# Kernel optimization log

Measured on AMD Instinct MI355X. Metric: run time of the kernel, lower is better.

Reference implementation:

```python
import jax, jax.numpy as jnp
import numpy as np

NUM_HEAD = 8
ATTN_DIM = 512
WINDOW_WIDTH = 31
HALF_WIN = WINDOW_WIDTH // 2  # symmetric band half-width
NEG_INF = -1e10


def setup_inputs() -> dict:
    key = jax.random.key(0)
    k0, k1, k2 = jax.random.split(key, 3)
    n, c, w = 4, 512, 2048
    out_dim = 512
    input_ = jax.random.normal(k0, (n, c, 1, w), dtype=jnp.float32)
    mask = jnp.ones((n, w), dtype=jnp.float32)  # 1 = valid key position
    # xavier-uniform-like init for the two linears, zero bias (as in the module)
    lim_in = np.sqrt(6.0 / (c + 3 * ATTN_DIM)).astype(np.float32)
    W_in = jax.random.uniform(k1, (3 * ATTN_DIM, c), jnp.float32, -lim_in, lim_in)
    b_in = jnp.zeros((3 * ATTN_DIM,), jnp.float32)
    lim_fc = np.sqrt(6.0 / (ATTN_DIM + out_dim)).astype(np.float32)
    W_fc = jax.random.uniform(k2, (out_dim, ATTN_DIM), jnp.float32, -lim_fc, lim_fc)
    b_fc = jnp.zeros((out_dim,), jnp.float32)
    return {"input_": input_, "mask": mask, "W_in": W_in, "b_in": b_in,
            "W_fc": W_fc, "b_fc": b_fc}


def reference(input_, mask, W_in, b_in, W_fc, b_fc):
    n, c, h, w = input_.shape  # h == 1
    d = ATTN_DIM // NUM_HEAD
    x = input_.reshape(n, c, w).transpose(0, 2, 1)          # [n, w, c]
    temp = x @ W_in.T + b_in                                # [n, w, 3A]
    temp = temp.transpose(0, 2, 1)                          # [n, 3A, w]
    # channel layout after chunk(num_head) then chunk(3): [h, {q,k,v}, d]
    qkv = temp.reshape(n, NUM_HEAD, 3, d, w)
    q, k, v = qkv[:, :, 0], qkv[:, :, 1], qkv[:, :, 2]      # each [n, H, d, w]
    scale = NUM_HEAD / ATTN_DIM                              # == 1/d_head
    attn = jnp.einsum('nhdi,nhdj->nhij', q, k) * scale       # [n, H, w, w]
    # windowed band mask combined with per-key padding mask (clip_mask/mha_mask)
    idx = jnp.arange(w)
    band = jnp.abs(idx[:, None] - idx[None, :]) <= HALF_WIN  # [w, w]
    valid = band[None, None, :, :] & (mask > 0.5)[:, None, None, :]
    attn = jnp.where(valid, attn, NEG_INF)                   # pre-softmax mask
    attn = jax.nn.softmax(attn, axis=-1)
    attn = jnp.where(valid, attn, 0.0)                       # post-softmax mask
    # dropout in eval mode (identity) for a deterministic reference
    out = jnp.einsum('nhdj,nhij->nhdi', v, attn)             # [n, H, d, w]
    out = out.reshape(n, ATTN_DIM, w).transpose(0, 2, 1)     # [n, w, A]
    out = out @ W_fc.T + b_fc                                # [n, w, out_dim]
    od = out.shape[-1]
    return out.transpose(0, 2, 1).reshape(n, od, 1, w)
```

## Files before the change

kernel.cpp:

```cpp
#include <hip/hip_runtime.h>
#include <hip/hip_bf16.h>
#include <math.h>

#define W_SEQ   2048
#define C_IN    512
#define N_BATCH 4
#define NHEAD   8
#define QKV_CH  1536
#define OUT_CH  512
#define ATTND   512
#define N1_4    (QKV_CH * C_IN / 4)
#define N2_4    (OUT_CH * ATTND / 4)

typedef __attribute__((ext_vector_type(8))) short bf16x8;
typedef __attribute__((ext_vector_type(8))) unsigned short u16x8;
typedef __attribute__((ext_vector_type(4))) float f32x4;

__device__ __forceinline__ void gld16(const void* g, void* l) {
    __builtin_amdgcn_global_load_lds((const __attribute__((address_space(1))) void*)g,
                                     (__attribute__((address_space(3))) void*)l, 16, 0, 0);
}
__device__ __forceinline__ unsigned short f2bf(float f) {
    unsigned u = __float_as_uint(f);
    return (unsigned short)((u + 0x7FFFu + ((u >> 16) & 1u)) >> 16);
}

__device__ __forceinline__ void grid_sync(unsigned* bar, unsigned target) {
    __syncthreads();
    if (threadIdx.x == 0) {
        __threadfence();
        atomicAdd(bar, 1u);
        while (atomicAdd(bar, 0u) < target)
            __builtin_amdgcn_s_sleep(8);
        __threadfence();
    }
    __syncthreads();
}

__device__ __forceinline__ void prep_unit(char* sm, int b,
    const float* __restrict__ input, unsigned short* __restrict__ Xh,
    const float* __restrict__ W_in, unsigned short* __restrict__ Winh,
    const float* __restrict__ W_fc, unsigned short* __restrict__ Wfch)
{
    const int t = threadIdx.x;
    float (*ts)[65] = (float(*)[65])sm;
    const int n  = b >> 8, rm = b & 255;
    const int i0 = (rm & 31) * 64, c0 = (rm >> 5) * 64;
    const int tx = t & 63, ty = t >> 6;
    #pragma unroll
    for (int s = 0; s < 16; ++s) {
        const int c = s * 4 + ty;
        ts[c][tx] = input[((size_t)(n * C_IN + c0 + c)) * W_SEQ + i0 + tx];
    }
    __syncthreads();
    const int c8 = t & 7, il = t >> 3;
    #pragma unroll
    for (int s = 0; s < 2; ++s) {
        const int i = il + 32 * s;
        u16x8 hv;
        #pragma unroll
        for (int e = 0; e < 8; ++e) hv[e] = f2bf(ts[c8 * 8 + e][i]);
        *(u16x8*)(&Xh[((size_t)(n * W_SEQ + i0 + i)) * C_IN + c0 + c8 * 8]) = hv;
    }
    const int idx = b * 256 + t;
    if (idx < N1_4) {
        const float4 v = ((const float4*)W_in)[idx];
        ushort4 hh; hh.x = f2bf(v.x); hh.y = f2bf(v.y); hh.z = f2bf(v.z); hh.w = f2bf(v.w);
        ((ushort4*)Winh)[idx] = hh;
    } else {
        const int j = idx - N1_4;
        const float4 v = ((const float4*)W_fc)[j];
        ushort4 hh; hh.x = f2bf(v.x); hh.y = f2bf(v.y); hh.z = f2bf(v.z); hh.w = f2bf(v.w);
        ((ushort4*)Wfch)[j] = hh;
    }
}

template<int EPI>
__device__ __forceinline__ void gemm_body(char* sm, int bx, int by,
    const unsigned short* __restrict__ A, const unsigned short* __restrict__ B,
    const float* __restrict__ bias, void* __restrict__ Cv, const int ldc)
{
    const int t = threadIdx.x;
    const int l = t & 63, w = t >> 6;
    const int m0 = by * 128, n0 = bx * 128;
    const int wm = w >> 1, wn = w & 1;

    const int subrow = l >> 3;
    const int swz    = ((l & 7) ^ subrow) << 4;
    const char* pA = (const char*)A + (size_t)m0 * 1024 + swz;
    const char* pB = (const char*)B + (size_t)n0 * 1024 + swz;

    const int frow = l & 15;
    f32x4 acc[4][4] = {};

    for (int k0 = 0; k0 < 512; k0 += 64) {
        const int kb = k0 * 2;
        #pragma unroll
        for (int c = 0; c < 4; ++c) {
            const int q = 4 * w + c;
            const size_t roff = (size_t)(q * 8 + subrow) * 1024 + kb;
            gld16(pA + roff, sm +         q * 1024);
            gld16(pB + roff, sm + 16384 + q * 1024);
        }
        __syncthreads();
        #pragma unroll
        for (int kk = 0; kk < 2; ++kk) {
            const int cswz = (kk * 64 + ((l >> 4) << 4)) ^ ((l & 7) << 4);
            bf16x8 a[4], b[4];
            #pragma unroll
            for (int mi = 0; mi < 4; ++mi)
                a[mi] = *(const bf16x8*)(sm + (wm * 64 + mi * 16 + frow) * 128 + cswz);
            #pragma unroll
            for (int ni = 0; ni < 4; ++ni)
                b[ni] = *(const bf16x8*)(sm + 16384 + (wn * 64 + ni * 16 + frow) * 128 + cswz);
            #pragma unroll
            for (int mi = 0; mi < 4; ++mi)
                #pragma unroll
                for (int ni = 0; ni < 4; ++ni)
                    acc[mi][ni] = __builtin_amdgcn_mfma_f32_16x16x32_bf16(a[mi], b[ni], acc[mi][ni], 0, 0, 0);
        }
        __syncthreads();
    }

    const int g = l >> 4;
    #pragma unroll
    for (int mi = 0; mi < 4; ++mi) {
        #pragma unroll
        for (int ni = 0; ni < 4; ++ni) {
            const int colg = n0 + wn * 64 + ni * 16 + frow;
            #pragma unroll
            for (int r = 0; r < 4; ++r) {
                const int rowg = m0 + wm * 64 + mi * 16 + g * 4 + r;
                const float v = acc[mi][ni][r];
                if (EPI == 0) {
                    ((unsigned short*)Cv)[(size_t)rowg * ldc + colg] = f2bf(v + bias[colg]);
                } else {
                    const int nb = colg >> 11, ii = colg & (W_SEQ - 1);
                    ((float*)Cv)[((size_t)(nb * OUT_CH + rowg)) * W_SEQ + ii] = v + bias[rowg];
                }
            }
        }
    }
}

#define VT_OFF  13824
#define MSK_OFF 30208

__device__ __forceinline__ void attn_body(char* sm, int blk,
    const unsigned short* __restrict__ qkv, const float* __restrict__ mask,
    unsigned short* __restrict__ aoh)
{
    const int t = threadIdx.x, l = t & 63, w = t >> 6;
    const int i0 = (blk & 31) * 64, h = (blk >> 5) & 7, n = blk >> 8;
    const int lr = l & 15, lg = l >> 4;

    const char* tb = (const char*)qkv + ((size_t)n * W_SEQ * QKV_CH + h * 192) * 2;

    const int r8 = l >> 3, c8 = l & 7;
    #pragma unroll
    for (int it = 0; it < 3; ++it) {
        const int jl = w * 24 + it * 8 + r8;
        const int jg = i0 - 16 + jl;
        bf16x8 kv = {}, vv = {};
        if (jg >= 0 && jg < W_SEQ) {
            const char* rp = tb + (size_t)jg * 3072;
            kv = *(const bf16x8*)(rp + 128 + c8 * 16);
            vv = *(const bf16x8*)(rp + 256 + c8 * 16);
        }
        *(bf16x8*)(sm + jl * 144 + c8 * 16) = kv;
        const int J0 = jl >> 3;
        #pragma unroll
        for (int e = 0; e < 8; ++e) {
            const int d = c8 * 8 + e;
            const int fold = ((d >> 3) ^ d) & 7;
            *(unsigned short*)(sm + VT_OFF + d * 256 + (((J0 ^ fold) << 4) | ((jl & 7) * 2)))
                = (unsigned short)vv[e];
        }
    }
    bf16x8 qh[2];
    {
        const char* qrow = tb + (size_t)(i0 + w * 16 + lr) * 3072 + lg * 16;
        qh[0] = *(const bf16x8*)(qrow);
        qh[1] = *(const bf16x8*)(qrow + 64);
    }
    if (t < 96) {
        const int jg = i0 - 16 + t;
        *(float*)(sm + MSK_OFF + t * 4) = (jg >= 0 && jg < W_SEQ) ? mask[n * W_SEQ + jg] : 0.f;
    }
    __syncthreads();

    f32x4 sacc[6] = {};
    #pragma unroll
    for (int nf = 0; nf < 6; ++nf) {
        #pragma unroll
        for (int kk = 0; kk < 2; ++kk) {
            const bf16x8 kh = *(const bf16x8*)(sm + (nf * 16 + lr) * 144 + kk * 64 + lg * 16);
            sacc[nf] = __builtin_amdgcn_mfma_f32_16x16x32_bf16(qh[kk], kh, sacc[nf], 0, 0, 0);
        }
    }
    __syncthreads();

    float mv[6];
    #pragma unroll
    for (int nf = 0; nf < 6; ++nf)
        mv[nf] = *(const float*)(sm + MSK_OFF + (nf * 16 + lr) * 4);

    #pragma unroll
    for (int r = 0; r < 4; ++r) {
        const int ri = w * 16 + lg * 4 + r;
        float sv[6], mrow = -1.0e30f;
        #pragma unroll
        for (int nf = 0; nf < 6; ++nf) {
            const int jcol = nf * 16 + lr;
            const bool valid = (jcol > ri) && (jcol <= ri + 31) && (mv[nf] > 0.5f);
            const float s = valid ? sacc[nf][r] * 0.015625f : -1.0e30f;
            sv[nf] = s;
            mrow = fmaxf(mrow, s);
        }
        #pragma unroll
        for (int off = 1; off <= 8; off <<= 1) mrow = fmaxf(mrow, __shfl_xor(mrow, off));
        float ls = 0.f;
        #pragma unroll
        for (int nf = 0; nf < 6; ++nf) {
            float pp = __expf(sv[nf] - mrow);
            pp = (sv[nf] > -1.0e29f) ? pp : 0.f;
            sv[nf] = pp;
            ls += pp;
        }
        #pragma unroll
        for (int off = 1; off <= 8; off <<= 1) ls += __shfl_xor(ls, off);
        const float rinv = (ls > 0.f) ? 1.f / ls : 0.f;
        #pragma unroll
        for (int nf = 0; nf < 6; ++nf)
            *(unsigned short*)(sm + ri * 208 + (nf * 16 + lr) * 2) = f2bf(sv[nf] * rinv);
    }

    f32x4 oacc[4] = {};
    #pragma unroll
    for (int ks = 0; ks < 3; ++ks) {
        const bf16x8 pah = *(const bf16x8*)(sm + (w * 16 + lr) * 208 + ks * 64 + lg * 16);
        #pragma unroll
        for (int nf2 = 0; nf2 < 4; ++nf2) {
            const int dd = nf2 * 16 + lr;
            const int fold = ((dd >> 3) ^ dd) & 7;
            const bf16x8 vb = *(const bf16x8*)(sm + VT_OFF + dd * 256 + (((4 * ks + lg) ^ fold) << 4));
            oacc[nf2] = __builtin_amdgcn_mfma_f32_16x16x32_bf16(pah, vb, oacc[nf2], 0, 0, 0);
        }
    }

    #pragma unroll
    for (int nf2 = 0; nf2 < 4; ++nf2) {
        #pragma unroll
        for (int r = 0; r < 4; ++r) {
            const int ri = w * 16 + lg * 4 + r;
            aoh[((size_t)(n * W_SEQ + i0 + ri)) * ATTND + h * 64 + nf2 * 16 + lr] = f2bf(oacc[nf2][r]);
        }
    }
}

__global__ __launch_bounds__(256, 4) void fused_all_k(
    const float* __restrict__ input, const float* __restrict__ mask,
    const float* __restrict__ W_in,  const float* __restrict__ b_in,
    const float* __restrict__ W_fc,  const float* __restrict__ b_fc,
    float* __restrict__ out,
    unsigned short* __restrict__ QKVh, unsigned short* __restrict__ AOh,
    unsigned short* __restrict__ Winh, unsigned short* __restrict__ Wfch,
    unsigned short* __restrict__ Xh, unsigned* __restrict__ bar)
{
    __shared__ __align__(16) char sm[32768];
    const int G = gridDim.x;

    for (int u = blockIdx.x; u < 1024; u += G) {
        prep_unit(sm, u, input, Xh, W_in, Winh, W_fc, Wfch);
        __syncthreads();
    }
    grid_sync(bar + 0, G);

    for (int u = blockIdx.x; u < 768; u += G) {
        const int y8 = u & 7, r = u >> 3;
        gemm_body<0>(sm, r % 12, (r / 12) * 8 + y8, Xh, Winh, b_in, QKVh, QKV_CH);
        __syncthreads();
    }
    grid_sync(bar + 16, G);

    for (int u = blockIdx.x; u < 1024; u += G) {
        attn_body(sm, u, QKVh, mask, AOh);
        __syncthreads();
    }
    grid_sync(bar + 32, G);

    for (int u = blockIdx.x; u < 256; u += G)
        gemm_body<1>(sm, u >> 2, u & 3, Wfch, AOh, b_fc, out, 0);
}

__global__ __launch_bounds__(256, 4) void prep_sep_k(
    const float* __restrict__ input, unsigned short* __restrict__ Xh,
    const float* __restrict__ W_in, unsigned short* __restrict__ Winh,
    const float* __restrict__ W_fc, unsigned short* __restrict__ Wfch)
{
    __shared__ __align__(16) char sm[32768];
    prep_unit(sm, blockIdx.x, input, Xh, W_in, Winh, W_fc, Wfch);
}
__global__ __launch_bounds__(256, 4) void gemm1_sep_k(
    const unsigned short* __restrict__ A, const unsigned short* __restrict__ B,
    const float* __restrict__ bias, unsigned short* __restrict__ C)
{
    __shared__ __align__(16) char sm[32768];
    const int d = blockIdx.x, y8 = d & 7, r = d >> 3;
    gemm_body<0>(sm, r % 12, (r / 12) * 8 + y8, A, B, bias, C, QKV_CH);
}
__global__ __launch_bounds__(256, 4) void attn_sep_k(
    const unsigned short* __restrict__ qkv, const float* __restrict__ mask,
    unsigned short* __restrict__ aoh)
{
    __shared__ __align__(16) char sm[32768];
    attn_body(sm, blockIdx.x, qkv, mask, aoh);
}
__global__ __launch_bounds__(256, 4) void gemm2_sep_k(
    const unsigned short* __restrict__ A, const unsigned short* __restrict__ B,
    const float* __restrict__ bias, float* __restrict__ out)
{
    __shared__ __align__(16) char sm[32768];
    gemm_body<1>(sm, blockIdx.x >> 2, blockIdx.x & 3, A, B, bias, out, 0);
}

extern "C" void kernel_launch(void* const* d_in, const int* in_sizes, int n_in,
                              void* d_out, int out_size, void* d_ws, size_t ws_size,
                              hipStream_t stream)
{
    const float* input = (const float*)d_in[0];
    const float* mask  = (const float*)d_in[1];
    const float* W_in  = (const float*)d_in[2];
    const float* b_in  = (const float*)d_in[3];
    const float* W_fc  = (const float*)d_in[4];
    const float* b_fc  = (const float*)d_in[5];
    float* out = (float*)d_out;
    char* ws = (char*)d_ws;

    unsigned short* QKVh = (unsigned short*)ws;
    unsigned short* AOh  = (unsigned short*)(ws + 25165824);
    unsigned short* Winh = (unsigned short*)(ws + 33554432);
    unsigned short* Wfch = (unsigned short*)(ws + 35127296);
    unsigned short* Xh   = (unsigned short*)(ws + 35651584);
    unsigned*       bar  = (unsigned*)(ws + 46137344);

    int occ = 0;
    hipOccupancyMaxActiveBlocksPerMultiprocessor(&occ, fused_all_k, 256, 0);

    if (occ >= 4) {
        hipMemsetAsync(bar, 0, 192, stream);
        fused_all_k<<<dim3(1024), 256, 0, stream>>>(
            input, mask, W_in, b_in, W_fc, b_fc, out,
            QKVh, AOh, Winh, Wfch, Xh, bar);
    } else {
        prep_sep_k <<<dim3(1024), 256, 0, stream>>>(input, Xh, W_in, Winh, W_fc, Wfch);
        gemm1_sep_k<<<dim3(768),  256, 0, stream>>>(Xh, Winh, b_in, QKVh);
        attn_sep_k <<<dim3(1024), 256, 0, stream>>>(QKVh, mask, AOh);
        gemm2_sep_k<<<dim3(256),  256, 0, stream>>>(Wfch, AOh, b_fc, out);
    }
}
```

Before: 50.44 us.

## Replace grid-wide barriers with tree barrier and per-tile dataflow flags

Replaces the single-counter grid barrier after the prep stage with a two-level tree barrier, so 1024 blocks do not all contend on one atomic. The two later grid barriers become fine-grained completion counters. Each attention block waits only on the QKV row tiles it reads, and each output-GEMM block waits only on the attention panel it consumes, so stages can overlap. This relies on all 1024 blocks being co-resident and on the flag indexing matching the tile mapping; a mismatch could deadlock or read stale data.

```diff
diff --git a/kernel.cpp b/kernel.cpp
--- a/kernel.cpp
+++ b/kernel.cpp
@@ -24,14 +24,21 @@
     unsigned u = __float_as_uint(f);
     return (unsigned short)((u + 0x7FFFu + ((u >> 16) & 1u)) >> 16);
 }
-
-__device__ __forceinline__ void grid_sync(unsigned* bar, unsigned target) {
+__device__ __forceinline__ unsigned ld_flag(const unsigned* p) {
+    return __hip_atomic_load(p, __ATOMIC_RELAXED, __HIP_MEMORY_SCOPE_AGENT);
+}
+
+__device__ __forceinline__ void tree_barrier(unsigned* flg) {
     __syncthreads();
     if (threadIdx.x == 0) {
         __threadfence();
-        atomicAdd(bar, 1u);
-        while (atomicAdd(bar, 0u) < target)
-            __builtin_amdgcn_s_sleep(8);
+        unsigned* leaf = flg + (blockIdx.x >> 4) * 16;
+        unsigned* root = flg + 1024;
+        unsigned* rel  = flg + 1040;
+        if (atomicAdd(leaf, 1u) == 15u)
+            if (atomicAdd(root, 1u) == 63u)
+                __hip_atomic_store(rel, 1u, __ATOMIC_RELEASE, __HIP_MEMORY_SCOPE_AGENT);
+        while (ld_flag(rel) == 0u) __builtin_amdgcn_s_sleep(2);
         __threadfence();
     }
     __syncthreads();
@@ -265,32 +272,56 @@
     float* __restrict__ out,
     unsigned short* __restrict__ QKVh, unsigned short* __restrict__ AOh,
     unsigned short* __restrict__ Winh, unsigned short* __restrict__ Wfch,
-    unsigned short* __restrict__ Xh, unsigned* __restrict__ bar)
-{
-    __shared__ __align__(16) char sm[32768];
-    const int G = gridDim.x;
-
-    for (int u = blockIdx.x; u < 1024; u += G) {
-        prep_unit(sm, u, input, Xh, W_in, Winh, W_fc, Wfch);
-        __syncthreads();
-    }
-    grid_sync(bar + 0, G);
-
-    for (int u = blockIdx.x; u < 768; u += G) {
-        const int y8 = u & 7, r = u >> 3;
-        gemm_body<0>(sm, r % 12, (r / 12) * 8 + y8, Xh, Winh, b_in, QKVh, QKV_CH);
-        __syncthreads();
-    }
-    grid_sync(bar + 16, G);
-
-    for (int u = blockIdx.x; u < 1024; u += G) {
-        attn_body(sm, u, QKVh, mask, AOh);
-        __syncthreads();
-    }
-    grid_sync(bar + 32, G);
-
-    for (int u = blockIdx.x; u < 256; u += G)
-        gemm_body<1>(sm, u >> 2, u & 3, Wfch, AOh, b_fc, out, 0);
+    unsigned short* __restrict__ Xh, unsigned* __restrict__ flg)
+{
+    __shared__ __align__(16) char sm[32768];
+    const int b = blockIdx.x;
+    unsigned* qdone = flg + 2048;
+    unsigned* adone = flg + 3072;
+
+    prep_unit(sm, b, input, Xh, W_in, Winh, W_fc, Wfch);
+    tree_barrier(flg);
+
+    if (b < 768) {
+        const int y8 = b & 7, r = b >> 3;
+        const int by = (r / 12) * 8 + y8;
+        gemm_body<0>(sm, r % 12, by, Xh, Winh, b_in, QKVh, QKV_CH);
+        __syncthreads();
+        if (threadIdx.x == 0) {
+            __threadfence();
+            atomicAdd(qdone + by * 16, 1u);
+        }
+    }
+
+    {
+        const int n = b >> 8, i0 = (b & 31) * 64;
+        const int row1 = n * W_SEQ + ((i0 >= 16) ? i0 - 16 : 0);
+        const int row2 = n * W_SEQ + ((i0 + 79 <= W_SEQ - 1) ? i0 + 79 : W_SEQ - 1);
+        const int t1 = row1 >> 7, t2 = row2 >> 7;
+        if (threadIdx.x == 0) {
+            while (ld_flag(qdone + t1 * 16) < 12u) __builtin_amdgcn_s_sleep(2);
+            while (ld_flag(qdone + t2 * 16) < 12u) __builtin_amdgcn_s_sleep(2);
+            __threadfence();
+        }
+        __syncthreads();
+        attn_body(sm, b, QKVh, mask, AOh);
+        __syncthreads();
+        if (threadIdx.x == 0) {
+            __threadfence();
+            const int panel = n * 16 + (i0 >> 7);
+            atomicAdd(adone + panel * 16, 1u);
+        }
+    }
+
+    if (b < 256) {
+        const int bx = b >> 2, by = b & 3;
+        if (threadIdx.x == 0) {
+            while (ld_flag(adone + bx * 16) < 16u) __builtin_amdgcn_s_sleep(2);
+            __threadfence();
+        }
+        __syncthreads();
+        gemm_body<1>(sm, bx, by, Wfch, AOh, b_fc, out, 0);
+    }
 }
 
 __global__ __launch_bounds__(256, 4) void prep_sep_k(
@@ -342,16 +373,16 @@
     unsigned short* Winh = (unsigned short*)(ws + 33554432);
     unsigned short* Wfch = (unsigned short*)(ws + 35127296);
     unsigned short* Xh   = (unsigned short*)(ws + 35651584);
-    unsigned*       bar  = (unsigned*)(ws + 46137344);
+    unsigned*       flg  = (unsigned*)(ws + 46137344);
 
     int occ = 0;
     hipOccupancyMaxActiveBlocksPerMultiprocessor(&occ, fused_all_k, 256, 0);
 
     if (occ >= 4) {
-        hipMemsetAsync(bar, 0, 192, stream);
+        hipMemsetAsync(flg, 0, 16384, stream);
         fused_all_k<<<dim3(1024), 256, 0, stream>>>(
             input, mask, W_in, b_in, W_fc, b_fc, out,
-            QKVh, AOh, Winh, Wfch, Xh, bar);
+            QKVh, AOh, Winh, Wfch, Xh, flg);
     } else {
         prep_sep_k <<<dim3(1024), 256, 0, stream>>>(input, Xh, W_in, Winh, W_fc, Wfch);
         gemm1_sep_k<<<dim3(768),  256, 0, stream>>>(Xh, Winh, b_in, QKVh);
```

After: 50.77 us (median of 2 runs). About the same (+0.7%).
